# Kernel tuning notes

Measured on AMD Instinct MI355X. Metric: run time of the kernel, lower is better.

Reference implementation:

```python
import jax, jax.numpy as jnp
import numpy as np

N, D, M = 500000, 32, 1000


def setup_inputs() -> dict:
    key = jax.random.key(0)
    k1, k2, k3, k4 = jax.random.split(key, 4)
    x = jax.random.normal(k1, (N, D), dtype=jnp.float32)
    score_p = jax.random.normal(k2, (N, D), dtype=jnp.float32)
    log_p = jax.random.normal(k3, (N,), dtype=jnp.float32)
    laplace_log_p = jax.random.normal(k4, (N,), dtype=jnp.float32)
    return {
        "x": x,
        "log_p": log_p,
        "score_p": score_p,
        "laplace_log_p": laplace_log_p,
        "lengthscale": jnp.float32(1.0),
        "m": M,
    }


def _stein_imq_row(xi, si, X, S, ell2, dim):
    # Langevin Stein kernel with IMQ base k(x,y) = (1 + ||x-y||^2/ell^2)^{-1/2},
    # evaluated between the pivot (xi, si) and ALL n points (X, S) at once.
    diff = xi[None, :] - X                      # (n, d)
    r2 = jnp.sum(diff * diff, axis=-1)          # (n,)
    q = 1.0 + r2 / ell2
    g = q ** -1.5
    # (s_i - s_j) . (x_i - x_j) / ell^2
    cross = (diff @ si - jnp.sum(S * diff, axis=-1)) / ell2
    # div_x div_y k + (sx . grad_y k + sy . grad_x k) + (sx . sy) k
    return (dim / ell2) * g - 3.0 * r2 / (ell2 * ell2) * q ** -2.5 + cross * g + (S @ si) * q ** -0.5


def reference(x, log_p, score_p, laplace_log_p, lengthscale, m):
    n, d = x.shape
    w = 1.0 / float(m)                           # weight_entropy default = 1/m
    ell2 = lengthscale * lengthscale
    # diagonal k_p(x_i, x_i) = d/ell^2 + ||s_i||^2 (diff=0, q=1)
    init_diag = d / ell2 + jnp.sum(score_p * score_p, axis=-1)
    obj0 = init_diag + laplace_log_p - w * log_p  # (n,)
    idx0 = jnp.argmin(obj0)

    def step(carry, _):
        obj, idx = carry
        ki = _stein_imq_row(x[idx], score_p[idx], x, score_p, ell2, d)
        obj = obj + 2.0 * ki - w * log_p
        new_idx = jnp.argmin(obj)
        return (obj, new_idx), new_idx

    (_, _), idx_tail = jax.lax.scan(step, (obj0, idx0), None, length=m - 1)
    return jnp.concatenate([idx0[None], idx_tail])
```

## Files before the change

### kernel.cpp

```cpp
#include <hip/hip_runtime.h>

#define BLOCK 512
#define GRID  256
#define PPT   4
#define V     8
#define V3    3
#define DIMS  32
#define SLOTS_PER_THREAD (GRID / 64)

__device__ __forceinline__ float to_agpr(float v) {
    float r;
    asm volatile("v_accvgpr_write_b32 %0, %1" : "=a"(r) : "v"(v));
    return r;
}
__device__ __forceinline__ float from_agpr(float a) {
    float r;
    asm volatile("v_accvgpr_read_b32 %0, %1" : "=v"(r) : "a"(a));
    return r;
}

__device__ __forceinline__ unsigned pack_f32(float v) {
    unsigned u = __float_as_uint(v);
    return (u & 0x80000000u) ? ~u : (u | 0x80000000u);
}

__device__ __forceinline__ unsigned long long pack_min(float v, unsigned idx) {
    return ((unsigned long long)pack_f32(v) << 32) | (unsigned long long)idx;
}

__device__ __forceinline__ unsigned long long shfl_down_u64(unsigned long long v, int off) {
    unsigned lo = (unsigned)(v & 0xffffffffu);
    unsigned hi = (unsigned)(v >> 32);
    lo = __shfl_down(lo, off, 64);
    hi = __shfl_down(hi, off, 64);
    return ((unsigned long long)hi << 32) | (unsigned long long)lo;
}

__device__ __forceinline__ unsigned long long shfl_xor_u64(unsigned long long v, int mask) {
    unsigned lo = (unsigned)(v & 0xffffffffu);
    unsigned hi = (unsigned)(v >> 32);
    lo = __shfl_xor(lo, mask, 64);
    hi = __shfl_xor(hi, mask, 64);
    return ((unsigned long long)hi << 32) | (unsigned long long)lo;
}

__device__ __forceinline__ unsigned long long block_min_reduce(unsigned long long v,
                                                              unsigned long long* scratch) {
    #pragma unroll
    for (int off = 32; off >= 1; off >>= 1) {
        unsigned long long o = shfl_down_u64(v, off);
        v = (o < v) ? o : v;
    }
    const int wave = threadIdx.x >> 6;
    const int lane = threadIdx.x & 63;
    if (lane == 0) scratch[wave] = v;
    __syncthreads();
    unsigned long long r = scratch[0];
    #pragma unroll
    for (int i = 1; i < (BLOCK / 64); ++i) {
        unsigned long long o = scratch[i];
        r = (o < r) ? o : r;
    }
    __syncthreads();
    return r;
}

__device__ __forceinline__ void post_slot(unsigned long long* __restrict__ slots,
                                          unsigned long long blockmin, int t) {
    if (threadIdx.x == 0) {
        const unsigned long long val = blockmin >> 32;
        const unsigned long long idx = blockmin & 0xFFFFFull;
        const unsigned long long key =
            (val << 32) | ((unsigned long long)((unsigned)t & 0xFFFu) << 20) | idx;
        __hip_atomic_store(&slots[(size_t)(t & 1) * GRID + blockIdx.x], key,
                           __ATOMIC_RELAXED, __HIP_MEMORY_SCOPE_AGENT);
    }
}

__device__ __forceinline__ void gather_min(
    const unsigned long long* __restrict__ slotp, int t,
    unsigned long long* gmin_sh)
{
    if (threadIdx.x < 64) {
        const unsigned want = (unsigned)t & 0xFFFu;
        unsigned long long k[SLOTS_PER_THREAD];
        for (;;) {
            #pragma unroll
            for (int s = 0; s < SLOTS_PER_THREAD; ++s)
                k[s] = __hip_atomic_load(&slotp[threadIdx.x + 64 * s],
                                         __ATOMIC_RELAXED, __HIP_MEMORY_SCOPE_AGENT);
            bool ok = true;
            #pragma unroll
            for (int s = 0; s < SLOTS_PER_THREAD; ++s)
                ok &= (((unsigned)(k[s] >> 20) & 0xFFFu) == want);
            if (ok) break;
        }
        unsigned long long lb = k[0];
        #pragma unroll
        for (int s = 1; s < SLOTS_PER_THREAD; ++s)
            if (k[s] < lb) lb = k[s];
        #pragma unroll
        for (int mask = 32; mask >= 1; mask >>= 1) {
            unsigned long long o = shfl_xor_u64(lb, mask);
            lb = (o < lb) ? o : lb;
        }
        if (threadIdx.x == 0) *gmin_sh = lb;
    }
    __syncthreads();
}

__global__
__attribute__((amdgpu_flat_work_group_size(512, 512),
               amdgpu_waves_per_eu(2, 2)))
void stein_thin_persist(
    const float* __restrict__ x, const float* __restrict__ log_p,
    const float* __restrict__ score_p, const float* __restrict__ laplace,
    const float* __restrict__ ls_ptr, int* __restrict__ out,
    unsigned long long* __restrict__ slots, int N, int m)
{
    const int tid = blockIdx.x * BLOCK + threadIdx.x;
    const int T = GRID * BLOCK;
    const int lane = threadIdx.x & 63;
    const int wave = threadIdx.x >> 6;

    const float ell = ls_ptr[0];
    const float ell2 = ell * ell;
    const float w = 1.0f / (float)m;
    const float dim_over_ell2 = (float)DIMS / ell2;
    const float inv_ell2 = 1.0f / ell2;
    const float inv2 = inv_ell2 * inv_ell2;

    const float4* __restrict__ X4 = (const float4*)x;
    const float4* __restrict__ S4 = (const float4*)score_p;

    __shared__ float4 s_ldsT[V][2 * BLOCK];
    __shared__ float4 s_lds3[V3][BLOCK];
    __shared__ unsigned long long gmin_sh;
    __shared__ unsigned long long red_scratch[BLOCK / 64];

    float4 xr0[V];
    float4 xr1[V];
    float ax2[DIMS], ax3[DIMS];
    float as2[DIMS], as3[(V - V3) * 4];
    float objr[PPT], lpr[PPT];

    {
        unsigned long long lbest = ~0ULL;
        #pragma unroll
        for (int p = 0; p < PPT; ++p) {
            const int j = tid + p * T;
            const bool act = (j < N);
            const int jc = act ? j : (N - 1);
            const size_t base = (size_t)jc * V;
            float ss = 0.0f;
            #pragma unroll
            for (int v = 0; v < V; ++v) {
                const float4 s = S4[base + v];
                if (p < 2) s_ldsT[v][p * BLOCK + threadIdx.x] = s;
                if (p == 2) {
                    as2[4 * v + 0] = to_agpr(s.x); as2[4 * v + 1] = to_agpr(s.y);
                    as2[4 * v + 2] = to_agpr(s.z); as2[4 * v + 3] = to_agpr(s.w);
                }
                if (p == 3) {
                    if (v < V3) s_lds3[v][threadIdx.x] = s;
                    else {
                        const int b = (v - V3) * 4;
                        as3[b + 0] = to_agpr(s.x); as3[b + 1] = to_agpr(s.y);
                        as3[b + 2] = to_agpr(s.z); as3[b + 3] = to_agpr(s.w);
                    }
                }
                const float4 xx = X4[base + v];
                if (p == 0) xr0[v] = xx;
                else if (p == 1) xr1[v] = xx;
                else if (p == 2) {
                    ax2[4 * v + 0] = to_agpr(xx.x); ax2[4 * v + 1] = to_agpr(xx.y);
                    ax2[4 * v + 2] = to_agpr(xx.z); ax2[4 * v + 3] = to_agpr(xx.w);
                } else {
                    ax3[4 * v + 0] = to_agpr(xx.x); ax3[4 * v + 1] = to_agpr(xx.y);
                    ax3[4 * v + 2] = to_agpr(xx.z); ax3[4 * v + 3] = to_agpr(xx.w);
                }
                ss += s.x * s.x; ss += s.y * s.y; ss += s.z * s.z; ss += s.w * s.w;
            }
            lpr[p] = log_p[jc];
            float o = ((dim_over_ell2 + ss) + laplace[jc]) - w * log_p[jc];
            if (!act) o = __int_as_float(0x7F800000);
            objr[p] = o;
            const unsigned long long pk = pack_min(o, (unsigned)j);
            if (pk < lbest) lbest = pk;
        }
        post_slot(slots, block_min_reduce(lbest, red_scratch), 0);
    }
    __syncthreads();

    for (int t = 1; t < m; ++t) {
        gather_min(slots + (size_t)((t - 1) & 1) * GRID, t - 1, &gmin_sh);
        const int pidx = (int)(gmin_sh & 0xFFFFFull);
        if (blockIdx.x == 0 && threadIdx.x == 0) out[t - 1] = pidx;
        const size_t pb = (size_t)pidx * V;

        float r2a[PPT], c1a[PPT], c2a[PPT], dssa[PPT];
        #pragma unroll
        for (int p = 0; p < PPT; ++p) {
            r2a[p] = 0.0f; c1a[p] = 0.0f; c2a[p] = 0.0f; dssa[p] = 0.0f;
        }

        #pragma unroll
        for (int v = 0; v < V; ++v) {
            const float4 xp = X4[pb + v];
            const float4 sp = S4[pb + v];
            #pragma unroll
            for (int p = 0; p < PPT; ++p) {
                float4 xv, sv;
                if (p == 0)      { xv = xr0[v]; sv = s_ldsT[v][threadIdx.x]; }
                else if (p == 1) { xv = xr1[v]; sv = s_ldsT[v][BLOCK + threadIdx.x]; }
                else if (p == 2) {
                    xv.x = from_agpr(ax2[4 * v + 0]); xv.y = from_agpr(ax2[4 * v + 1]);
                    xv.z = from_agpr(ax2[4 * v + 2]); xv.w = from_agpr(ax2[4 * v + 3]);
                    sv.x = from_agpr(as2[4 * v + 0]); sv.y = from_agpr(as2[4 * v + 1]);
                    sv.z = from_agpr(as2[4 * v + 2]); sv.w = from_agpr(as2[4 * v + 3]);
                } else {
                    xv.x = from_agpr(ax3[4 * v + 0]); xv.y = from_agpr(ax3[4 * v + 1]);
                    xv.z = from_agpr(ax3[4 * v + 2]); xv.w = from_agpr(ax3[4 * v + 3]);
                    if (v < V3) sv = s_lds3[v][threadIdx.x];
                    else {
                        const int b = (v - V3) * 4;
                        sv.x = from_agpr(as3[b + 0]); sv.y = from_agpr(as3[b + 1]);
                        sv.z = from_agpr(as3[b + 2]); sv.w = from_agpr(as3[b + 3]);
                    }
                }
                float d;
                d = xp.x - xv.x; r2a[p] += d * d; c1a[p] += d * sp.x; c2a[p] += sv.x * d; dssa[p] += sv.x * sp.x;
                d = xp.y - xv.y; r2a[p] += d * d; c1a[p] += d * sp.y; c2a[p] += sv.y * d; dssa[p] += sv.y * sp.y;
                d = xp.z - xv.z; r2a[p] += d * d; c1a[p] += d * sp.z; c2a[p] += sv.z * d; dssa[p] += sv.z * sp.z;
                d = xp.w - xv.w; r2a[p] += d * d; c1a[p] += d * sp.w; c2a[p] += sv.w * d; dssa[p] += sv.w * sp.w;
            }
        }

        unsigned long long lbest = ~0ULL;
        #pragma unroll
        for (int p = 0; p < PPT; ++p) {
            const float r2 = r2a[p];
            const float q   = 1.0f + r2 * inv_ell2;
            const float qi  = 1.0f / q;
            const float sq  = sqrtf(qi);
            const float g   = qi * sq;
            const float q25 = qi * qi * sq;
            const float cross = (c1a[p] - c2a[p]) * inv_ell2;
            const float k = ((dim_over_ell2 * g - 3.0f * r2 * inv2 * q25)
                             + cross * g) + dssa[p] * sq;
            const float o = objr[p] + (2.0f * k - w * lpr[p]);
            objr[p] = o;
            const unsigned long long pk = pack_min(o, (unsigned)(tid + p * T));
            if (pk < lbest) lbest = pk;
        }

        #pragma unroll
        for (int off = 32; off >= 1; off >>= 1) {
            unsigned long long o = shfl_down_u64(lbest, off);
            lbest = (o < lbest) ? o : lbest;
        }
        if (lane == 0) red_scratch[wave] = lbest;
        __syncthreads();
        if (threadIdx.x == 0) {
            unsigned long long r = red_scratch[0];
            #pragma unroll
            for (int i = 1; i < (BLOCK / 64); ++i) {
                unsigned long long o = red_scratch[i];
                r = (o < r) ? o : r;
            }
            post_slot(slots, r, t);
        }
    }

    {
        gather_min(slots + (size_t)((m - 1) & 1) * GRID, m - 1, &gmin_sh);
        if (blockIdx.x == 0 && threadIdx.x == 0)
            out[m - 1] = (int)(gmin_sh & 0xFFFFFull);
    }
}

extern "C" void kernel_launch(void* const* d_in, const int* in_sizes, int n_in,
                              void* d_out, int out_size, void* d_ws, size_t ws_size,
                              hipStream_t stream) {
    const float* x        = (const float*)d_in[0];
    const float* log_p    = (const float*)d_in[1];
    const float* score_p  = (const float*)d_in[2];
    const float* laplace  = (const float*)d_in[3];
    const float* ls_ptr   = (const float*)d_in[4];

    int* out = (int*)d_out;
    int N = in_sizes[1];
    int m = out_size;

    unsigned long long* slots = (unsigned long long*)d_ws;

    stein_thin_persist<<<dim3(GRID), dim3(BLOCK), 0, stream>>>(
        x, log_p, score_p, laplace, ls_ptr, out, slots, N, m);
}
```

Before: 6.055 ms.

## Remove block barriers: every wave polls global slots and last-arriving wave posts block min

Each wave now polls the global per-block slots and reduces the grid minimum on its own, so the shared-memory broadcast and its __syncthreads are gone. The block-level reduction uses an LDS ticket counter: the last wave to arrive combines the per-wave partials and posts the block key, replacing the second barrier. This removes two block-wide barriers per iteration in exchange for 8x more global polling traffic per block. It also relies on LDS ordering between the partial writes and the ticket atomic without an explicit fence, which may be a race.

```diff
diff --git a/kernel.cpp b/kernel.cpp
--- a/kernel.cpp
+++ b/kernel.cpp
@@ -7,6 +7,7 @@
 #define V3    3
 #define DIMS  32
 #define SLOTS_PER_THREAD (GRID / 64)
+#define NWAVES (BLOCK / 64)
 
 __device__ __forceinline__ float to_agpr(float v) {
     float r;
@@ -57,7 +58,7 @@
     __syncthreads();
     unsigned long long r = scratch[0];
     #pragma unroll
-    for (int i = 1; i < (BLOCK / 64); ++i) {
+    for (int i = 1; i < NWAVES; ++i) {
         unsigned long long o = scratch[i];
         r = (o < r) ? o : r;
     }
@@ -65,48 +66,42 @@
     return r;
 }
 
-__device__ __forceinline__ void post_slot(unsigned long long* __restrict__ slots,
-                                          unsigned long long blockmin, int t) {
-    if (threadIdx.x == 0) {
-        const unsigned long long val = blockmin >> 32;
-        const unsigned long long idx = blockmin & 0xFFFFFull;
-        const unsigned long long key =
-            (val << 32) | ((unsigned long long)((unsigned)t & 0xFFFu) << 20) | idx;
-        __hip_atomic_store(&slots[(size_t)(t & 1) * GRID + blockIdx.x], key,
-                           __ATOMIC_RELAXED, __HIP_MEMORY_SCOPE_AGENT);
-    }
-}
-
-__device__ __forceinline__ void gather_min(
-    const unsigned long long* __restrict__ slotp, int t,
-    unsigned long long* gmin_sh)
-{
-    if (threadIdx.x < 64) {
-        const unsigned want = (unsigned)t & 0xFFFu;
-        unsigned long long k[SLOTS_PER_THREAD];
-        for (;;) {
-            #pragma unroll
-            for (int s = 0; s < SLOTS_PER_THREAD; ++s)
-                k[s] = __hip_atomic_load(&slotp[threadIdx.x + 64 * s],
-                                         __ATOMIC_RELAXED, __HIP_MEMORY_SCOPE_AGENT);
-            bool ok = true;
-            #pragma unroll
-            for (int s = 0; s < SLOTS_PER_THREAD; ++s)
-                ok &= (((unsigned)(k[s] >> 20) & 0xFFFu) == want);
-            if (ok) break;
-        }
-        unsigned long long lb = k[0];
-        #pragma unroll
-        for (int s = 1; s < SLOTS_PER_THREAD; ++s)
-            if (k[s] < lb) lb = k[s];
-        #pragma unroll
-        for (int mask = 32; mask >= 1; mask >>= 1) {
-            unsigned long long o = shfl_xor_u64(lb, mask);
-            lb = (o < lb) ? o : lb;
-        }
-        if (threadIdx.x == 0) *gmin_sh = lb;
-    }
-    __syncthreads();
+__device__ __forceinline__ void post_key(unsigned long long* __restrict__ slots,
+                                         unsigned long long blockmin, int t, int bid) {
+    const unsigned long long val = blockmin >> 32;
+    const unsigned long long idx = blockmin & 0xFFFFFull;
+    const unsigned long long key =
+        (val << 32) | ((unsigned long long)((unsigned)t & 0xFFFu) << 20) | idx;
+    __hip_atomic_store(&slots[(size_t)(t & 1) * GRID + bid], key,
+                       __ATOMIC_RELAXED, __HIP_MEMORY_SCOPE_AGENT);
+}
+
+__device__ __forceinline__ unsigned long long gather_all(
+    const unsigned long long* __restrict__ slotp, int t) {
+    const int lane = threadIdx.x & 63;
+    const unsigned want = (unsigned)t & 0xFFFu;
+    unsigned long long k[SLOTS_PER_THREAD];
+    for (;;) {
+        #pragma unroll
+        for (int s = 0; s < SLOTS_PER_THREAD; ++s)
+            k[s] = __hip_atomic_load(&slotp[lane + 64 * s],
+                                     __ATOMIC_RELAXED, __HIP_MEMORY_SCOPE_AGENT);
+        bool ok = true;
+        #pragma unroll
+        for (int s = 0; s < SLOTS_PER_THREAD; ++s)
+            ok &= (((unsigned)(k[s] >> 20) & 0xFFFu) == want);
+        if (ok) break;
+    }
+    unsigned long long lb = k[0];
+    #pragma unroll
+    for (int s = 1; s < SLOTS_PER_THREAD; ++s)
+        if (k[s] < lb) lb = k[s];
+    #pragma unroll
+    for (int mask = 32; mask >= 1; mask >>= 1) {
+        unsigned long long o = shfl_xor_u64(lb, mask);
+        lb = (o < lb) ? o : lb;
+    }
+    return lb;
 }
 
 __global__
@@ -135,14 +130,17 @@
 
     __shared__ float4 s_ldsT[V][2 * BLOCK];
     __shared__ float4 s_lds3[V3][BLOCK];
-    __shared__ unsigned long long gmin_sh;
-    __shared__ unsigned long long red_scratch[BLOCK / 64];
+    __shared__ unsigned long long red_scratch[NWAVES];
+    __shared__ unsigned long long part[NWAVES];
+    __shared__ int ticket[2];
 
     float4 xr0[V];
     float4 xr1[V];
     float ax2[DIMS], ax3[DIMS];
     float as2[DIMS], as3[(V - V3) * 4];
     float objr[PPT], lpr[PPT];
+
+    if (threadIdx.x == 0) { ticket[0] = 0; ticket[1] = 0; }
 
     {
         unsigned long long lbest = ~0ULL;
@@ -188,13 +186,15 @@
             const unsigned long long pk = pack_min(o, (unsigned)j);
             if (pk < lbest) lbest = pk;
         }
-        post_slot(slots, block_min_reduce(lbest, red_scratch), 0);
+        const unsigned long long r0 = block_min_reduce(lbest, red_scratch);
+        if (threadIdx.x == 0) post_key(slots, r0, 0, blockIdx.x);
     }
     __syncthreads();
 
     for (int t = 1; t < m; ++t) {
-        gather_min(slots + (size_t)((t - 1) & 1) * GRID, t - 1, &gmin_sh);
-        const int pidx = (int)(gmin_sh & 0xFFFFFull);
+        const unsigned long long gmin =
+            gather_all(slots + (size_t)((t - 1) & 1) * GRID, t - 1);
+        const int pidx = (int)(gmin & 0xFFFFFull);
         if (blockIdx.x == 0 && threadIdx.x == 0) out[t - 1] = pidx;
         const size_t pb = (size_t)pidx * V;
 
@@ -259,23 +259,27 @@
             unsigned long long o = shfl_down_u64(lbest, off);
             lbest = (o < lbest) ? o : lbest;
         }
-        if (lane == 0) red_scratch[wave] = lbest;
-        __syncthreads();
-        if (threadIdx.x == 0) {
-            unsigned long long r = red_scratch[0];
-            #pragma unroll
-            for (int i = 1; i < (BLOCK / 64); ++i) {
-                unsigned long long o = red_scratch[i];
-                r = (o < r) ? o : r;
+        if (lane == 0) {
+            part[wave] = lbest;
+            const int old = atomicAdd(&ticket[t & 1], 1);
+            if (old == NWAVES - 1) {
+                unsigned long long r = part[0];
+                #pragma unroll
+                for (int i = 1; i < NWAVES; ++i) {
+                    unsigned long long o = part[i];
+                    r = (o < r) ? o : r;
+                }
+                post_key(slots, r, t, blockIdx.x);
+                ticket[t & 1] = 0;
             }
-            post_slot(slots, r, t);
         }
     }
 
     {
-        gather_min(slots + (size_t)((m - 1) & 1) * GRID, m - 1, &gmin_sh);
+        const unsigned long long gmin =
+            gather_all(slots + (size_t)((m - 1) & 1) * GRID, m - 1);
         if (blockIdx.x == 0 && threadIdx.x == 0)
-            out[m - 1] = (int)(gmin_sh & 0xFFFFFull);
+            out[m - 1] = (int)(gmin & 0xFFFFFull);
     }
 }
 
```

Measured after the change: 10.03 ms. +65.6%, slower.
